# Kernel tuning notes

Hardware: AMD Instinct MI355X
Metric: run time of the kernel (lower is better)

The kernel has to match this reference:

```python
import jax, jax.numpy as jnp
import numpy as np

B, S, D, R = 4, 4096, 1024, 128
EPS_MAG = 1e-8
EPS_LN = 1e-5


def setup_inputs() -> dict:
    key = jax.random.key(0)
    ks = jax.random.split(key, 24)
    w = lambda k, shape, s=0.02: (jax.random.normal(k, shape, jnp.float32) * s)
    d = {}
    d["x"] = jax.random.normal(ks[0], (B, S, D), jnp.float32)
    d["W_dt_down"] = w(ks[1], (D, R))            # dt_proj_down (no bias)
    d["W_dt_up"] = w(ks[2], (R, D))
    d["b_dt_up"] = jnp.full((D,), -4.0, jnp.float32)  # nn.init.constant_(-4.0)
    d["W_gate"] = w(ks[3], (D, D)); d["b_gate"] = jnp.zeros((D,), jnp.float32)
    d["W_phi1"] = w(ks[4], (D, D)); d["b_phi1"] = jnp.zeros((D,), jnp.float32)
    d["W_phi2"] = w(ks[5], (D, D)); d["b_phi2"] = jnp.zeros((D,), jnp.float32)
    d["omega_base"] = jax.random.normal(ks[6], (D,), jnp.float32) * 0.1
    d["W_omega"] = w(ks[7], (D, D)); d["b_omega"] = jnp.zeros((D,), jnp.float32)
    d["W_mag"] = w(ks[8], (D, D)); d["b_mag"] = jnp.zeros((D,), jnp.float32)
    d["W_qoff"] = w(ks[9], (D, D)); d["b_qoff"] = jnp.zeros((D,), jnp.float32)
    d["ln_g"] = jnp.ones((2 * D,), jnp.float32); d["ln_b"] = jnp.zeros((2 * D,), jnp.float32)
    d["W_out1"] = w(ks[10], (2 * D, D)); d["b_out1"] = jnp.zeros((D,), jnp.float32)
    d["W_out2"] = w(ks[11], (D, D)); d["b_out2"] = jnp.zeros((D,), jnp.float32)
    return d


def _forward(x, W_dt_down, W_dt_up, b_dt_up, W_gate, b_gate, W_phi1, b_phi1,
             W_phi2, b_phi2, omega_base, W_omega, b_omega, W_mag, b_mag,
             W_qoff, b_qoff, ln_g, ln_b, W_out1, b_out1, W_out2, b_out2):
    h = x  # expand_factor == 1 -> in_proj is Identity
    # input-dependent delta (low-rank)
    dt = jax.nn.softplus((h @ W_dt_down) @ W_dt_up + b_dt_up)        # [B,S,D]
    select_gate = jax.nn.sigmoid(h @ W_gate + b_gate)
    omega = omega_base + (h @ W_omega + b_omega)
    omega_scaled = omega * dt * 0.01
    phi_init = jax.nn.gelu(h @ W_phi1 + b_phi1, approximate=False) @ W_phi2 + b_phi2
    phi = phi_init + jnp.cumsum(omega_scaled, axis=1)                # phase accumulation
    magnitude = jax.nn.sigmoid(h @ W_mag + b_mag) * 5.0
    content = select_gate * h * magnitude
    memory_real = jnp.cumsum(content * jnp.cos(phi), axis=1)
    memory_imag = jnp.cumsum(content * jnp.sin(phi), axis=1)
    acc_mag = jnp.cumsum(magnitude * select_gate, axis=1)
    sqrt_mag = jnp.sqrt(acc_mag + EPS_MAG)
    mr = memory_real / sqrt_mag
    mi = memory_imag / sqrt_mag
    # rotation-based retrieval
    phi_q = phi + (h @ W_qoff + b_qoff)
    cq, sq = jnp.cos(phi_q), jnp.sin(phi_q)
    retrieved_real = mr * cq + mi * sq
    retrieved_imag = mi * cq - mr * sq
    ctx = jnp.concatenate([retrieved_real, retrieved_imag], axis=-1)  # [B,S,2D]
    mu = jnp.mean(ctx, axis=-1, keepdims=True)
    var = jnp.mean((ctx - mu) ** 2, axis=-1, keepdims=True)
    ln = (ctx - mu) / jnp.sqrt(var + EPS_LN) * ln_g + ln_b
    out = jax.nn.gelu(ln @ W_out1 + b_out1, approximate=False) @ W_out2 + b_out2
    return x + out


def reference(x, W_dt_down, W_dt_up, b_dt_up, W_gate, b_gate, W_phi1, b_phi1,
              W_phi2, b_phi2, omega_base, W_omega, b_omega, W_mag, b_mag,
              W_qoff, b_qoff, ln_g, ln_b, W_out1, b_out1, W_out2, b_out2):
    return _forward(x, W_dt_down, W_dt_up, b_dt_up, W_gate, b_gate, W_phi1, b_phi1,
                    W_phi2, b_phi2, omega_base, W_omega, b_omega, W_mag, b_mag,
                    W_qoff, b_qoff, ln_g, ln_b, W_out1, b_out1, W_out2, b_out2)
```

## Files before the change

### kernel.cpp

```cpp
#include <hip/hip_runtime.h>


#define D_ 1024
#define S_ 4096
#define MQ 4096
#define MF 16384
#define CHUNK 64
#define NCH (S_/CHUNK)

typedef float f32x4 __attribute__((ext_vector_type(4)));
typedef __bf16 bf16x8 __attribute__((ext_vector_type(8)));
typedef short s16x8 __attribute__((ext_vector_type(8)));

typedef __attribute__((address_space(1))) void gvoid;
typedef __attribute__((address_space(3))) void lvoid;

__device__ __forceinline__ void g2l16(const void* g, void* l) {
  __builtin_amdgcn_global_load_lds((gvoid*)g, (lvoid*)l, 16, 0, 0);
}

__device__ __forceinline__ float bflo(unsigned int w){ union{unsigned int i; float f;} c; c.i = w<<16; return c.f; }
__device__ __forceinline__ float bfhi(unsigned int w){ union{unsigned int i; float f;} c; c.i = w & 0xFFFF0000u; return c.f; }
__device__ __forceinline__ unsigned short f2bf(float f){
  union{float f; unsigned int i;} c; c.f=f;
  unsigned int u = c.i + 0x7FFFu + ((c.i>>16)&1u);
  return (unsigned short)(u>>16);
}
__device__ __forceinline__ unsigned int pack2(float lo, float hi){
  return (unsigned int)f2bf(lo) | ((unsigned int)f2bf(hi)<<16);
}

__device__ __forceinline__ float sig_(float x){ return 1.f/(1.f+__expf(-x)); }
__device__ __forceinline__ float gelu_(float x){ return 0.5f*x*(1.f+erff(x*0.70710678118654752440f)); }
__device__ __forceinline__ float softplus_(float x){ return (x>0.f) ? x + log1pf(__expf(-x)) : log1pf(__expf(x)); }

template<int MODE>
__global__ __launch_bounds__(256)
void gemmF(const unsigned short* __restrict__ A0,
           const unsigned short* __restrict__ A1,
           const unsigned short* __restrict__ B0,
           const unsigned short* __restrict__ B1,
           const float* __restrict__ bias0,
           const float* __restrict__ bias1,
           const float* __restrict__ extra,
           unsigned short* __restrict__ out0,
           unsigned short* __restrict__ out1,
           float* __restrict__ outf)
{
  __shared__ unsigned short As[128*32];
  __shared__ unsigned short Bs[128*32];
  const int tid = threadIdx.x;
  const int m0 = blockIdx.x * 128;
  const int n0 = blockIdx.y * 128;
  const int lane = tid & 63;
  const int wv = tid >> 6;
  const int wr = wv >> 1, wc = wv & 1;
  const int fr = lane & 15, fg = lane >> 4;

  const int r0 = tid >> 2;
  const int r1 = (tid + 256) >> 2;
  const int k8 = (tid & 3) * 8;

  const unsigned short* Ap; const unsigned short* Bp;
  int lda, ldb, K, brow0;
  if constexpr (MODE == 0)      { Ap=A0; lda=1024; K=1024; Bp=B0; ldb=1024; brow0=n0; }
  else if constexpr (MODE == 2) { Ap=A0; lda=2048; K=2048; Bp=B0; ldb=2048; brow0=n0; }
  else if constexpr (MODE == 3) { Ap=A0; lda=1024; K=1024; Bp=B0; ldb=1024; brow0=n0; }
  else {
    if (n0 < 1024) { Ap=A0; lda=1024; K=1024; Bp=B0; ldb=1024; brow0=n0; }
    else           { Ap=A1; lda=128;  K=128;  Bp=B1; ldb=128;  brow0=n0-1024; }
  }

  f32x4 acc[4][4];
#pragma unroll
  for (int i=0;i<4;i++)
#pragma unroll
    for (int j=0;j<4;j++)
#pragma unroll
      for (int q=0;q<4;q++) acc[i][j][q] = 0.f;

  for (int k0 = 0; k0 < K; k0 += 32) {
    __syncthreads();
    g2l16(Ap + (size_t)(m0+r0)*lda + k0 + k8, As + (size_t)tid*8);
    g2l16(Ap + (size_t)(m0+r1)*lda + k0 + k8, As + (size_t)(tid+256)*8);
    g2l16(Bp + (size_t)(brow0+r0)*ldb + k0 + k8, Bs + (size_t)tid*8);
    g2l16(Bp + (size_t)(brow0+r1)*ldb + k0 + k8, Bs + (size_t)(tid+256)*8);
    __syncthreads();

    s16x8 af[4], bfr[4];
#pragma unroll
    for (int mf=0; mf<4; mf++) af[mf]  = *(const s16x8*)&As[(wr*64 + mf*16 + fr)*32 + fg*8];
#pragma unroll
    for (int nf=0; nf<4; nf++) bfr[nf] = *(const s16x8*)&Bs[(wc*64 + nf*16 + fr)*32 + fg*8];
#pragma unroll
    for (int mf=0; mf<4; mf++)
#pragma unroll
      for (int nf=0; nf<4; nf++)
        acc[mf][nf] = __builtin_amdgcn_mfma_f32_16x16x32_bf16(
          __builtin_bit_cast(bf16x8, af[mf]), __builtin_bit_cast(bf16x8, bfr[nf]),
          acc[mf][nf], 0, 0, 0);
  }

  const int slice = n0 >> 10;
#pragma unroll
  for (int mf=0; mf<4; mf++) {
#pragma unroll
    for (int nf=0; nf<4; nf++) {
      const int gn = n0 + wc*64 + nf*16 + fr;
      float bv;
      if constexpr (MODE == 1) bv = (n0 < 1024) ? bias0[gn] : bias1[gn-1024];
      else bv = bias0[gn];
#pragma unroll
      for (int q=0; q<4; q++) {
        const int gm = m0 + wr*64 + mf*16 + fg*4 + q;
        const float z = acc[mf][nf][q] + bv;
        if constexpr (MODE == 0) {
          if (slice < 5) {
            const float r = (slice==0) ? sig_(z)
                          : (slice==2) ? gelu_(z)
                          : (slice==3) ? sig_(z)*5.f : z;
            out0[(size_t)slice*MQ*1024 + (size_t)gm*1024 + (gn&1023)] = f2bf(r);
          } else {
            out1[(size_t)gm*128 + (gn-5120)] = f2bf(z);
          }
        } else if constexpr (MODE == 1) {
          if (slice == 0) out0[(size_t)gm*1024 + gn] = f2bf(z);
          else            out1[(size_t)gm*1024 + (gn-1024)] = f2bf(softplus_(z));
        } else if constexpr (MODE == 2) {
          out0[(size_t)gm*1024 + gn] = f2bf(gelu_(z));
        } else {
          const size_t idx = (size_t)gm*1024 + gn;
          outf[idx] = z + extra[idx];
        }
      }
    }
  }
}

__global__ __launch_bounds__(256)
void cvtx_k(const float* __restrict__ x, unsigned int* __restrict__ hb)
{
  const size_t i = (size_t)blockIdx.x*256 + threadIdx.x;
  const float4 v = *(const float4*)(x + i*4);
  hb[i*2]   = pack2(v.x, v.y);
  hb[i*2+1] = pack2(v.z, v.w);
}

__global__ __launch_bounds__(256)
void tconv_k(const float* __restrict__ W, unsigned short* __restrict__ Wt, int K, int N)
{
  __shared__ float tile[32][33];
  const int kb = blockIdx.x*32, nb = blockIdx.y*32;
  const int tx = threadIdx.x & 31, ty = threadIdx.x >> 5;
#pragma unroll
  for (int i=0;i<32;i+=8) tile[ty+i][tx] = W[(size_t)(kb+ty+i)*N + (nb+tx)];
  __syncthreads();
#pragma unroll
  for (int i=0;i<32;i+=8) Wt[(size_t)(nb+ty+i)*K + (kb+tx)] = f2bf(tile[tx][ty+i]);
}

struct P7 { const float* s[7]; unsigned short* d[7]; };
__global__ __launch_bounds__(256)
void tconv7_k(P7 p)
{
  __shared__ float tile[32][33];
  const float* W = p.s[blockIdx.z];
  unsigned short* Wt = p.d[blockIdx.z];
  const int kb = blockIdx.x*32, nb = blockIdx.y*32;
  const int tx = threadIdx.x & 31, ty = threadIdx.x >> 5;
#pragma unroll
  for (int i=0;i<32;i+=8) tile[ty+i][tx] = W[(size_t)(kb+ty+i)*1024 + (nb+tx)];
  __syncthreads();
#pragma unroll
  for (int i=0;i<32;i+=8) Wt[(size_t)(nb+ty+i)*1024 + (kb+tx)] = f2bf(tile[tx][ty+i]);
}

__global__ __launch_bounds__(256)
void biascat_k(const float* bg, const float* bo, const float* ob, const float* bp1,
               const float* bm, const float* bq, float* bc)
{
  const int i = blockIdx.x*256 + threadIdx.x;
  if (i >= 5248) return;
  const int s = i >> 10, d = i & 1023;
  float v;
  if (s==0) v = bg[d];
  else if (s==1) v = bo[d] + ob[d];
  else if (s==2) v = bp1[d];
  else if (s==3) v = bm[d];
  else if (s==4) v = bq[d];
  else v = 0.f;
  bc[i] = v;
}

__global__ __launch_bounds__(256)
void scan1_k(unsigned int* __restrict__ zgate, unsigned int* __restrict__ zmag,
             unsigned int* __restrict__ zomega, const unsigned int* __restrict__ zdt,
             const unsigned int* __restrict__ hb,
             float* __restrict__ sumPhi, float* __restrict__ sumGm)
{
  const int flat = blockIdx.x*256 + threadIdx.x;
  const int dh = flat & 511;
  const int bc = flat >> 9;
  size_t i = (size_t)bc*CHUNK*(D_/2) + dh;
  float sp0=0,sp1=0,sg0=0,sg1=0;
  for (int s=0;s<CHUNK;s++,i+=D_/2) {
    const unsigned ga=zgate[i], mg=zmag[i], om=zomega[i], dt=zdt[i], hh=hb[i];
    const float ga0=bflo(ga), ga1=bfhi(ga), mg0=bflo(mg), mg1=bfhi(mg);
    const float od0 = bflo(om)*bflo(dt)*0.01f, od1 = bfhi(om)*bfhi(dt)*0.01f;
    const unsigned odp = pack2(od0, od1);
    zomega[i] = odp;
    sp0 += bflo(odp); sp1 += bfhi(odp);
    const float g0 = ga0*mg0, g1 = ga1*mg1;
    const unsigned gmp = pack2(g0, g1);
    zmag[i] = gmp;
    sg0 += bflo(gmp); sg1 += bfhi(gmp);
    zgate[i] = pack2(g0*bflo(hh), g1*bfhi(hh));
  }
  const int sidx = bc*D_ + dh*2;
  sumPhi[sidx]=sp0; sumPhi[sidx+1]=sp1;
  sumGm[sidx]=sg0;  sumGm[sidx+1]=sg1;
}

__global__ __launch_bounds__(256)
void scan2_k(float* __restrict__ a, float* __restrict__ b)
{
  const int chain = (blockIdx.x*256 + threadIdx.x) >> 6;
  const int lane  = threadIdx.x & 63;
  const size_t i = (size_t)lane*D_ + chain;
  const float v = a[i], w = b[i];
  float vi = v, wi = w;
#pragma unroll
  for (int off=1; off<64; off<<=1) {
    const float t = __shfl_up(vi, off, 64);
    const float u = __shfl_up(wi, off, 64);
    if (lane >= off) { vi += t; wi += u; }
  }
  a[i] = vi - v;
  b[i] = wi - w;
}

__global__ __launch_bounds__(256)
void scan3_k(const unsigned int* __restrict__ omdt, const unsigned int* __restrict__ content,
             const unsigned int* __restrict__ phinit, const float* __restrict__ phiOff,
             float* __restrict__ sumRe, float* __restrict__ sumIm)
{
  const int flat = blockIdx.x*256 + threadIdx.x;
  const int dh = flat & 511;
  const int bc = flat >> 9;
  size_t i = (size_t)bc*CHUNK*(D_/2) + dh;
  const int sidx = bc*D_ + dh*2;
  float p0 = phiOff[sidx], p1 = phiOff[sidx+1];
  float re0=0,re1=0,im0=0,im1=0;
  for (int s=0;s<CHUNK;s++,i+=D_/2) {
    const unsigned od = omdt[i], ct = content[i], pi = phinit[i];
    p0 += bflo(od); p1 += bfhi(od);
    const float phi0 = bflo(pi)+p0, phi1 = bfhi(pi)+p1;
    float s0,c0,s1,c1;
    __sincosf(phi0,&s0,&c0);
    __sincosf(phi1,&s1,&c1);
    const float ct0=bflo(ct), ct1=bfhi(ct);
    re0 += ct0*c0; im0 += ct0*s0;
    re1 += ct1*c1; im1 += ct1*s1;
  }
  sumRe[sidx]=re0; sumRe[sidx+1]=re1;
  sumIm[sidx]=im0; sumIm[sidx+1]=im1;
}

__global__ __launch_bounds__(256)
void scan5_k(const unsigned int* __restrict__ omdt, const unsigned int* __restrict__ content,
             const unsigned int* __restrict__ phinit, const unsigned int* __restrict__ gm,
             const unsigned int* __restrict__ qoff,
             const float* __restrict__ phiOff, const float* __restrict__ gmOff,
             const float* __restrict__ reOff, const float* __restrict__ imOff,
             unsigned int* __restrict__ ctx)
{
  const int flat = blockIdx.x*256 + threadIdx.x;
  const int dh = flat & 511;
  const int bc = flat >> 9;
  size_t i = (size_t)bc*CHUNK*(D_/2) + dh;
  const int sidx = bc*D_ + dh*2;
  float p0 = phiOff[sidx], p1 = phiOff[sidx+1];
  float ag0 = gmOff[sidx], ag1 = gmOff[sidx+1];
  float re0 = reOff[sidx], re1 = reOff[sidx+1];
  float im0 = imOff[sidx], im1 = imOff[sidx+1];
  const int mtok0 = bc*CHUNK;
  for (int s=0;s<CHUNK;s++,i+=D_/2) {
    const unsigned od = omdt[i], ct = content[i], pi = phinit[i], gq = gm[i], qo = qoff[i];
    p0 += bflo(od); p1 += bfhi(od);
    const float phi0 = bflo(pi)+p0, phi1 = bfhi(pi)+p1;
    float sn0,cs0,sn1,cs1;
    __sincosf(phi0,&sn0,&cs0);
    __sincosf(phi1,&sn1,&cs1);
    const float ct0=bflo(ct), ct1=bfhi(ct);
    re0 += ct0*cs0; im0 += ct0*sn0;
    re1 += ct1*cs1; im1 += ct1*sn1;
    ag0 += bflo(gq); ag1 += bfhi(gq);
    const float inv0 = rsqrtf(ag0 + 1e-8f), inv1 = rsqrtf(ag1 + 1e-8f);
    const float mr0 = re0*inv0, mi0 = im0*inv0;
    const float mr1 = re1*inv1, mi1 = im1*inv1;
    const float pq0 = phi0 + bflo(qo), pq1 = phi1 + bfhi(qo);
    float sq0,cq0,sq1,cq1;
    __sincosf(pq0,&sq0,&cq0);
    __sincosf(pq1,&sq1,&cq1);
    const size_t cb = (size_t)(mtok0+s)*D_ + dh;
    ctx[cb]        = pack2(mr0*cq0 + mi0*sq0, mr1*cq1 + mi1*sq1);
    ctx[cb + D_/2] = pack2(mi0*cq0 - mr0*sq0, mi1*cq1 - mr1*sq1);
  }
}

__global__ __launch_bounds__(256)
void ln_k(unsigned int* __restrict__ ctx, const float* __restrict__ gam, const float* __restrict__ bet)
{
  const int m = blockIdx.x, tid = threadIdx.x;
  const size_t base = (size_t)m*1024 + tid*4;
  const uint4 t = *(const uint4*)(ctx + base);
  float v[8] = { bflo(t.x), bfhi(t.x), bflo(t.y), bfhi(t.y),
                 bflo(t.z), bfhi(t.z), bflo(t.w), bfhi(t.w) };
  float s=0.f, ss=0.f;
#pragma unroll
  for (int j=0;j<8;j++){ s+=v[j]; ss+=v[j]*v[j]; }
  for (int o=32;o;o>>=1){ s += __shfl_xor(s,o); ss += __shfl_xor(ss,o); }
  __shared__ float red[8];
  const int wv = tid>>6, lane = tid&63;
  if (lane==0){ red[wv]=s; red[4+wv]=ss; }
  __syncthreads();
  s  = red[0]+red[1]+red[2]+red[3];
  ss = red[4]+red[5]+red[6]+red[7];
  const float mu = s*(1.f/2048.f);
  const float rstd = rsqrtf(ss*(1.f/2048.f) - mu*mu + 1e-5f);
  const int col = tid*8;
  float o[8];
#pragma unroll
  for (int j=0;j<8;j++) o[j] = (v[j]-mu)*rstd*gam[col+j] + bet[col+j];
  uint4 w;
  w.x = pack2(o[0],o[1]); w.y = pack2(o[2],o[3]);
  w.z = pack2(o[4],o[5]); w.w = pack2(o[6],o[7]);
  *(uint4*)(ctx + base) = w;
}

extern "C" void kernel_launch(void* const* d_in, const int* in_sizes, int n_in,
                              void* d_out, int out_size, void* d_ws, size_t ws_size,
                              hipStream_t stream)
{
  const float* x     = (const float*)d_in[0];
  const float* Wdd   = (const float*)d_in[1];
  const float* Wdu   = (const float*)d_in[2];
  const float* bdu   = (const float*)d_in[3];
  const float* Wg    = (const float*)d_in[4];
  const float* bg    = (const float*)d_in[5];
  const float* Wp1   = (const float*)d_in[6];
  const float* bp1   = (const float*)d_in[7];
  const float* Wp2   = (const float*)d_in[8];
  const float* bp2   = (const float*)d_in[9];
  const float* obase = (const float*)d_in[10];
  const float* Wo    = (const float*)d_in[11];
  const float* bo    = (const float*)d_in[12];
  const float* Wm    = (const float*)d_in[13];
  const float* bm    = (const float*)d_in[14];
  const float* Wq    = (const float*)d_in[15];
  const float* bq    = (const float*)d_in[16];
  const float* lng   = (const float*)d_in[17];
  const float* lnb   = (const float*)d_in[18];
  const float* Wo1   = (const float*)d_in[19];
  const float* bo1   = (const float*)d_in[20];
  const float* Wo2   = (const float*)d_in[21];
  const float* bo2   = (const float*)d_in[22];

  char* basep = (char*)d_ws;
  size_t off = 0;
  auto alloc = [&](size_t n) { char* q = basep + off; off = (off + n + 255) & ~(size_t)255; return q; };

  unsigned short* ctxF = (unsigned short*)alloc((size_t)MF*2048*2);
  char* qbase = alloc((size_t)5*MQ*1024*2 + (size_t)2*MQ*1024*2
                      + (size_t)MQ*1024*2 + (size_t)MQ*128*2);
  unsigned short* cat1 = (unsigned short*)qbase;
  unsigned short* cat2 = cat1 + (size_t)5*MQ*1024;
  unsigned short* hb   = cat2 + (size_t)2*MQ*1024;
  unsigned short* t1   = hb   + (size_t)MQ*1024;
  unsigned short* a3   = (unsigned short*)qbase;
  unsigned short* wt_cat = (unsigned short*)alloc((size_t)5248*1024*2);
  unsigned short* wt_p2  = (unsigned short*)alloc(1024*1024*2);
  unsigned short* wt_du  = (unsigned short*)alloc(1024*128*2);
  unsigned short* wt_o1  = (unsigned short*)alloc((size_t)1024*2048*2);
  unsigned short* wt_o2  = (unsigned short*)alloc(1024*1024*2);
  float* bias_cat = (float*)alloc(5248*4);
  float* sumPhi = (float*)alloc((size_t)NCH*D_*4);
  float* sumGm  = (float*)alloc((size_t)NCH*D_*4);
  float* sumRe  = (float*)alloc((size_t)NCH*D_*4);
  float* sumIm  = (float*)alloc((size_t)NCH*D_*4);

  const dim3 blk(256);

  P7 p7;
  p7.s[0]=Wg;  p7.d[0]=wt_cat + (size_t)0*1024*1024;
  p7.s[1]=Wo;  p7.d[1]=wt_cat + (size_t)1*1024*1024;
  p7.s[2]=Wp1; p7.d[2]=wt_cat + (size_t)2*1024*1024;
  p7.s[3]=Wm;  p7.d[3]=wt_cat + (size_t)3*1024*1024;
  p7.s[4]=Wq;  p7.d[4]=wt_cat + (size_t)4*1024*1024;
  p7.s[5]=Wp2; p7.d[5]=wt_p2;
  p7.s[6]=Wo2; p7.d[6]=wt_o2;
  tconv7_k<<<dim3(32,32,7), blk, 0, stream>>>(p7);
  tconv_k<<<dim3(32,4),  blk, 0, stream>>>(Wdd, wt_cat + (size_t)5120*1024, 1024,128);
  tconv_k<<<dim3(4,32),  blk, 0, stream>>>(Wdu, wt_du, 128,1024);
  tconv_k<<<dim3(64,32), blk, 0, stream>>>(Wo1, wt_o1, 2048,1024);
  biascat_k<<<21, blk, 0, stream>>>(bg, bo, obase, bp1, bm, bq, bias_cat);

  unsigned short* zgate  = cat1;
  unsigned short* zomega = cat1 + (size_t)1*MQ*1024;
  unsigned short* zphi1  = cat1 + (size_t)2*MQ*1024;
  unsigned short* zmag   = cat1 + (size_t)3*MQ*1024;
  unsigned short* zqoff  = cat1 + (size_t)4*MQ*1024;
  unsigned short* zpin   = cat2;
  unsigned short* zdt    = cat2 + (size_t)1*MQ*1024;

  for (int q = 0; q < 4; q++) {
    const float* xq = x + (size_t)q*MQ*D_;

    cvtx_k<<<MQ*D_/1024, blk, 0, stream>>>(xq, (unsigned int*)hb);

    gemmF<0><<<dim3(MQ/128, 41), blk, 0, stream>>>(hb, nullptr, wt_cat, nullptr,
                                                   bias_cat, nullptr, nullptr,
                                                   cat1, t1, nullptr);
    gemmF<1><<<dim3(MQ/128, 16), blk, 0, stream>>>(zphi1, t1, wt_p2, wt_du,
                                                   bp2, bdu, nullptr,
                                                   zpin, zdt, nullptr);
    scan1_k<<<128, blk, 0, stream>>>((unsigned int*)zgate,(unsigned int*)zmag,(unsigned int*)zomega,
                                     (const unsigned int*)zdt,(const unsigned int*)hb, sumPhi, sumGm);
    scan2_k<<<256, blk, 0, stream>>>(sumPhi, sumGm);
    scan3_k<<<128, blk, 0, stream>>>((const unsigned int*)zomega,(const unsigned int*)zgate,
                                     (const unsigned int*)zpin, sumPhi, sumRe, sumIm);
    scan2_k<<<256, blk, 0, stream>>>(sumRe, sumIm);
    scan5_k<<<128, blk, 0, stream>>>((const unsigned int*)zomega,(const unsigned int*)zgate,
                                     (const unsigned int*)zpin,(const unsigned int*)zmag,
                                     (const unsigned int*)zqoff,
                                     sumPhi, sumGm, sumRe, sumIm,
                                     (unsigned int*)ctxF + (size_t)q*MQ*1024);
  }

  ln_k<<<MF, blk, 0, stream>>>((unsigned int*)ctxF, lng, lnb);
  gemmF<2><<<dim3(MF/128, 8), blk, 0, stream>>>(ctxF, nullptr, wt_o1, nullptr,
                                                bo1, nullptr, nullptr,
                                                a3, nullptr, nullptr);
  gemmF<3><<<dim3(MF/128, 8), blk, 0, stream>>>(a3, nullptr, wt_o2, nullptr,
                                                bo2, nullptr, x,
                                                nullptr, nullptr, (float*)d_out);
}
```

Before: 931.5 us.

## Double-buffer LDS tiles in bf16 GEMM to overlap loads with MFMA

Switches the GEMM K-loop to two LDS buffers for A and B. It prefetches the next K tile via global_load_lds while MFMAs run on the current tile, and keeps one barrier per iteration instead of two. This aims to hide global-memory latency behind compute. LDS use doubles to 32KB per block, which may lower occupancy. Correctness depends on the single barrier and on the async LDS loads having completed by then.

```diff
diff --git a/kernel.cpp b/kernel.cpp
--- a/kernel.cpp
+++ b/kernel.cpp
@@ -47,8 +47,8 @@
            unsigned short* __restrict__ out1,
            float* __restrict__ outf)
 {
-  __shared__ unsigned short As[128*32];
-  __shared__ unsigned short Bs[128*32];
+  __shared__ unsigned short As[2][128*32];
+  __shared__ unsigned short Bs[2][128*32];
   const int tid = threadIdx.x;
   const int m0 = blockIdx.x * 128;
   const int n0 = blockIdx.y * 128;
@@ -71,6 +71,11 @@
     else           { Ap=A1; lda=128;  K=128;  Bp=B1; ldb=128;  brow0=n0-1024; }
   }
 
+  const unsigned short* ArowA = Ap + (size_t)(m0+r0)*lda + k8;
+  const unsigned short* ArowB = Ap + (size_t)(m0+r1)*lda + k8;
+  const unsigned short* BrowA = Bp + (size_t)(brow0+r0)*ldb + k8;
+  const unsigned short* BrowB = Bp + (size_t)(brow0+r1)*ldb + k8;
+
   f32x4 acc[4][4];
 #pragma unroll
   for (int i=0;i<4;i++)
@@ -79,19 +84,28 @@
 #pragma unroll
       for (int q=0;q<4;q++) acc[i][j][q] = 0.f;
 
-  for (int k0 = 0; k0 < K; k0 += 32) {
-    __syncthreads();
-    g2l16(Ap + (size_t)(m0+r0)*lda + k0 + k8, As + (size_t)tid*8);
-    g2l16(Ap + (size_t)(m0+r1)*lda + k0 + k8, As + (size_t)(tid+256)*8);
-    g2l16(Bp + (size_t)(brow0+r0)*ldb + k0 + k8, Bs + (size_t)tid*8);
-    g2l16(Bp + (size_t)(brow0+r1)*ldb + k0 + k8, Bs + (size_t)(tid+256)*8);
-    __syncthreads();
+  g2l16(ArowA + 0, &As[0][(size_t)tid*8]);
+  g2l16(ArowB + 0, &As[0][(size_t)(tid+256)*8]);
+  g2l16(BrowA + 0, &Bs[0][(size_t)tid*8]);
+  g2l16(BrowB + 0, &Bs[0][(size_t)(tid+256)*8]);
+  __syncthreads();
+
+  const int nt = K >> 5;
+  int cur = 0;
+  for (int t = 0; t < nt; ++t) {
+    if (t + 1 < nt) {
+      const int k0 = (t + 1) << 5;
+      g2l16(ArowA + k0, &As[cur^1][(size_t)tid*8]);
+      g2l16(ArowB + k0, &As[cur^1][(size_t)(tid+256)*8]);
+      g2l16(BrowA + k0, &Bs[cur^1][(size_t)tid*8]);
+      g2l16(BrowB + k0, &Bs[cur^1][(size_t)(tid+256)*8]);
+    }
 
     s16x8 af[4], bfr[4];
 #pragma unroll
-    for (int mf=0; mf<4; mf++) af[mf]  = *(const s16x8*)&As[(wr*64 + mf*16 + fr)*32 + fg*8];
-#pragma unroll
-    for (int nf=0; nf<4; nf++) bfr[nf] = *(const s16x8*)&Bs[(wc*64 + nf*16 + fr)*32 + fg*8];
+    for (int mf=0; mf<4; mf++) af[mf]  = *(const s16x8*)&As[cur][(wr*64 + mf*16 + fr)*32 + fg*8];
+#pragma unroll
+    for (int nf=0; nf<4; nf++) bfr[nf] = *(const s16x8*)&Bs[cur][(wc*64 + nf*16 + fr)*32 + fg*8];
 #pragma unroll
     for (int mf=0; mf<4; mf++)
 #pragma unroll
@@ -99,6 +113,9 @@
         acc[mf][nf] = __builtin_amdgcn_mfma_f32_16x16x32_bf16(
           __builtin_bit_cast(bf16x8, af[mf]), __builtin_bit_cast(bf16x8, bfr[nf]),
           acc[mf][nf], 0, 0, 0);
+
+    __syncthreads();
+    cur ^= 1;
   }
 
   const int slice = n0 >> 10;
```

Result: slower. 983.4 us (+5.6%).
